# Performance work log

Hardware: AMD Instinct MI355X
Metric: run time of the kernel (lower is better)

Reference implementation:

```python
import jax, jax.numpy as jnp
import numpy as np

N_NODES = 20000
N_EDGES = 200000
D_MODEL = 128
N_HEADS = 8
N_LAYERS = 2  # num_gnn - 1 concat layers


def setup_inputs() -> dict:
    key = jax.random.key(0)
    ks = jax.random.split(key, 12)
    s = 0.05  # keep activations well-scaled across residual layers
    hd = D_MODEL // N_HEADS  # 16
    return {
        "x": jax.random.normal(ks[0], (N_NODES, D_MODEL), jnp.float32),
        "src": jax.random.randint(ks[1], (N_EDGES,), 0, N_NODES),
        "dst": jax.random.randint(ks[2], (N_EDGES,), 0, N_NODES),
        "Ws": jax.random.normal(ks[3], (N_LAYERS, D_MODEL, D_MODEL), jnp.float32) * s,
        "als": jax.random.normal(ks[4], (N_LAYERS, N_HEADS, hd), jnp.float32) * s,
        "ars": jax.random.normal(ks[5], (N_LAYERS, N_HEADS, hd), jnp.float32) * s,
        "bs": jax.random.normal(ks[6], (N_LAYERS, D_MODEL), jnp.float32) * s,
        "W_last": jax.random.normal(ks[7], (D_MODEL, N_HEADS * D_MODEL), jnp.float32) * s,
        "al_last": jax.random.normal(ks[8], (N_HEADS, D_MODEL), jnp.float32) * s,
        "ar_last": jax.random.normal(ks[9], (N_HEADS, D_MODEL), jnp.float32) * s,
        "b_last": jax.random.normal(ks[10], (N_HEADS * D_MODEL,), jnp.float32) * s,
    }


def gat_conv(h, src, dst, W, al, ar, b, num_nodes):
    """DGL GATConv (eval mode, dropout off): returns (N, H, D) head outputs."""
    H, D = al.shape
    feat = (h @ W).reshape(num_nodes, H, D)          # (N,H,D)
    el = jnp.sum(feat * al[None], axis=-1)           # (N,H) attn on src side
    er = jnp.sum(feat * ar[None], axis=-1)           # (N,H) attn on dst side
    e = jax.nn.leaky_relu(el[src] + er[dst], 0.2)    # (E,H)
    # edge softmax over incoming edges of each dst node, per head
    m = jax.ops.segment_max(e, dst, num_segments=num_nodes)  # (N,H)
    p = jnp.exp(e - m[dst])                          # (E,H)
    z = jax.ops.segment_sum(p, dst, num_segments=num_nodes)  # (N,H)
    a = p / z[dst]                                   # (E,H)
    msg = feat[src] * a[..., None]                   # (E,H,D) weighted messages
    rst = jax.ops.segment_sum(msg, dst, num_segments=num_nodes)  # (N,H,D)
    return rst + b.reshape(1, H, D)


def reference(x, src, dst, Ws, als, ars, bs, W_last, al_last, ar_last, b_last):
    N = x.shape[0]
    h = x
    for i in range(N_LAYERS):
        temp = gat_conv(h, src, dst, Ws[i], als[i], ars[i], bs[i], N)  # (N,H,hd)
        h = h + jax.nn.elu(temp.reshape(N, -1))       # concat heads, ELU, residual
    temp = gat_conv(h, src, dst, W_last, al_last, ar_last, b_last, N)  # (N,H,D)
    h = h + jnp.mean(temp, axis=1)                    # mean over heads, residual
    return h
```

## Files before the change

kernel.cpp:

```cpp
#include <hip/hip_runtime.h>
#include <math.h>

#define N_NODES 20000
#define N_EDGES 200000
#define DM 128
#define NH 8

typedef __attribute__((ext_vector_type(8))) short bf16x8;
typedef __attribute__((ext_vector_type(4))) float f32x4;

__device__ __forceinline__ unsigned short f2b(float f) {
  unsigned int u = __float_as_uint(f);
  unsigned int r = (u + 0x7FFFu + ((u >> 16) & 1u)) >> 16;
  return (unsigned short)r;
}
__device__ __forceinline__ float b2f(unsigned short s) {
  return __uint_as_float(((unsigned int)s) << 16);
}

__global__ void scan_deg(const int* __restrict__ deg, int* __restrict__ off,
                         int* __restrict__ cursor) {
  __shared__ int part[1024];
  const int tid = threadIdx.x;
  const int CHUNK = (N_NODES + 1023) / 1024;
  int base = tid * CHUNK;
  int s = 0;
  for (int i = 0; i < CHUNK; ++i) {
    int idx = base + i;
    if (idx < N_NODES) s += deg[idx];
  }
  part[tid] = s;
  __syncthreads();
  for (int ofs = 1; ofs < 1024; ofs <<= 1) {
    int v = (tid >= ofs) ? part[tid - ofs] : 0;
    __syncthreads();
    part[tid] += v;
    __syncthreads();
  }
  int run = (tid > 0) ? part[tid - 1] : 0;
  for (int i = 0; i < CHUNK; ++i) {
    int idx = base + i;
    if (idx < N_NODES) {
      off[idx] = run;
      cursor[idx] = run;
      run += deg[idx];
    }
  }
  if (tid == 0) off[N_NODES] = part[1023];
}

__global__ void scatter_e(const int* __restrict__ src, const int* __restrict__ dst,
                          int* __restrict__ cursor, int* __restrict__ csr_src) {
  int e = blockIdx.x * blockDim.x + threadIdx.x;
  if (e < N_EDGES) {
    int p = atomicAdd(&cursor[dst[e]], 1);
    csr_src[p] = src[e];
  }
}

__global__ void prep_all(const float* __restrict__ x, float* __restrict__ h,
                         unsigned short* __restrict__ hb, const int* __restrict__ dst,
                         int* __restrict__ deg, const float* __restrict__ Ws,
                         unsigned short* __restrict__ wsz, const float* __restrict__ W_last,
                         unsigned short* __restrict__ wpsz, const float* __restrict__ al_last,
                         const float* __restrict__ ar_last, const float* __restrict__ b_last,
                         unsigned short* __restrict__ wlrsz, float* __restrict__ mb) {
  int i = blockIdx.x * blockDim.x + threadIdx.x;
  if (i < N_NODES * DM) {
    float v = x[i];
    h[i] = v;
    hb[i] = f2b(v);
  }
  if (i < N_EDGES) atomicAdd(&deg[dst[i]], 1);
  if (i < 2 * 16384) {
    int layer = i >> 14;
    int r = i & 16383;
    int j = r & 7, l = (r >> 3) & 63, f = (r >> 9) & 7, ks = r >> 12;
    int k = ks * 32 + ((l >> 4) << 3) + j;
    int n = f * 16 + (l & 15);
    wsz[i] = f2b(Ws[(size_t)layer * 16384 + k * 128 + n]);
  }
  if (i < 131072) {
    int j = i & 7, l = (i >> 3) & 63, f = (i >> 9) & 7, ks = i >> 12;
    int k = ks * 32 + ((l >> 4) << 3) + j;
    int n = f * 16 + (l & 15);
    int h_ = k >> 7, ko = k & 127;
    wpsz[i] = f2b(W_last[(size_t)ko * 1024 + h_ * 128 + n] * 0.125f);
  }
  if (i < 2048) {
    int j = i & 7, l = (i >> 3) & 63, ks = i >> 9;
    int k = ks * 32 + ((l >> 4) << 3) + j;
    int n = l & 15;
    int hh = n & 7;
    const float* av = (n < 8) ? (al_last + hh * 128) : (ar_last + hh * 128);
    float s = 0.f;
    for (int d = 0; d < 128; ++d) s += W_last[(size_t)k * 1024 + hh * 128 + d] * av[d];
    wlrsz[i] = f2b(s);
  }
  if (i < 128) {
    float s = 0.f;
#pragma unroll
    for (int hh = 0; hh < 8; ++hh) s += b_last[hh * 128 + i];
    mb[i] = s * 0.125f;
  }
}

template <int K, bool LAST>
__global__ __launch_bounds__(256) void gemm_mfma(
    const unsigned short* __restrict__ A, const unsigned short* __restrict__ Bsz,
    const float* __restrict__ hres, const float* __restrict__ mb,
    unsigned short* __restrict__ Cb, float* __restrict__ Cf,
    const float* __restrict__ al, const float* __restrict__ ar,
    float* __restrict__ elr) {
  const int tid = threadIdx.x;
  const int lane = tid & 63;
  const int wid = tid >> 6;
  const int wrow = wid & 1, wc = wid >> 1;
  const int r0 = blockIdx.x * 32;
  const int arow = r0 + wrow * 16 + (lane & 15);
  const int kg = lane >> 4;

  f32x4 acc[4];
#pragma unroll
  for (int fi = 0; fi < 4; ++fi) acc[fi] = {0.f, 0.f, 0.f, 0.f};

  const bf16x8* Ap = (const bf16x8*)(A + (size_t)arow * K + kg * 8);
  for (int ks = 0; ks < K / 32; ++ks) {
    bf16x8 a = Ap[ks * 4];
#pragma unroll
    for (int fi = 0; fi < 4; ++fi) {
      int f = wc * 4 + fi;
      bf16x8 b = *(const bf16x8*)(Bsz + (((size_t)(ks * 8 + f) * 64 + lane) << 3));
      acc[fi] = __builtin_amdgcn_mfma_f32_16x16x32_bf16(a, b, acc[fi], 0, 0, 0);
    }
  }

  const int rbase = r0 + wrow * 16 + (lane >> 4) * 4;
#pragma unroll
  for (int fi = 0; fi < 4; ++fi) {
    int col = wc * 64 + fi * 16 + (lane & 15);
#pragma unroll
    for (int r = 0; r < 4; ++r) {
      int row = rbase + r;
      float v = acc[fi][r];
      if (LAST)
        Cf[(size_t)row * DM + col] = v + hres[(size_t)row * DM + col] + mb[col];
      else
        Cb[(size_t)row * DM + col] = f2b(v);
    }
  }

  if (!LAST) {
#pragma unroll
    for (int fi = 0; fi < 4; ++fi) {
      int hh = wc * 4 + fi;
      float alv = al[hh * 16 + (lane & 15)];
      float arv = ar[hh * 16 + (lane & 15)];
#pragma unroll
      for (int r = 0; r < 4; ++r) {
        float pl = acc[fi][r] * alv;
        float pr = acc[fi][r] * arv;
#pragma unroll
        for (int msk = 1; msk < 16; msk <<= 1) {
          pl += __shfl_xor(pl, msk, 64);
          pr += __shfl_xor(pr, msk, 64);
        }
        if ((lane & 15) == 0) {
          int row = rbase + r;
          elr[row * 16 + hh] = pl;
          elr[row * 16 + 8 + hh] = pr;
        }
      }
    }
  }
}

__global__ __launch_bounds__(256) void elr_last(const unsigned short* __restrict__ hb,
                                                const unsigned short* __restrict__ wlrsz,
                                                float* __restrict__ elr) {
  const int lane = threadIdx.x & 63;
  const int wid = threadIdx.x >> 6;
  const int r0 = blockIdx.x * 64 + wid * 16;
  const int arow = r0 + (lane & 15);
  const int kg = lane >> 4;
  f32x4 acc = {0.f, 0.f, 0.f, 0.f};
  int arowc = arow < N_NODES ? arow : N_NODES - 1;
  const bf16x8* Ap = (const bf16x8*)(hb + (size_t)arowc * 128 + kg * 8);
#pragma unroll
  for (int ks = 0; ks < 4; ++ks) {
    bf16x8 a = Ap[ks * 4];
    bf16x8 b = *(const bf16x8*)(wlrsz + (((size_t)ks * 64 + lane) << 3));
    acc = __builtin_amdgcn_mfma_f32_16x16x32_bf16(a, b, acc, 0, 0, 0);
  }
  const int col = lane & 15;
  const int rbase = r0 + (lane >> 4) * 4;
#pragma unroll
  for (int r = 0; r < 4; ++r) {
    int row = rbase + r;
    if (row < N_NODES) elr[row * 16 + col] = acc[r];
  }
}

__global__ __launch_bounds__(256) void fused_small(
    const int* __restrict__ off, const int* __restrict__ csr_src,
    const unsigned short* __restrict__ feat, const float* __restrict__ elr,
    const float* __restrict__ bias, float* __restrict__ h, unsigned short* __restrict__ hb) {
  __shared__ float a_lds[4][64];
  __shared__ int s_lds[4][8];
  __shared__ float zi_lds[4][8];
  const int wid = threadIdx.x >> 6;
  const int t = blockIdx.x * 4 + wid;
  const int lane = threadIdx.x & 63;
  const int e_loc = lane >> 3, hh = lane & 7;
  const int h0 = lane >> 4;
  const int beg = off[t], end = off[t + 1];
  const float ert = elr[t * 16 + 8 + hh];

  float z = 0.f, acc0 = 0.f, acc1 = 0.f;
  for (int base = beg; base < end; base += 8) {
    int e = base + e_loc;
    int s = 0;
    float ex = 0.f;
    if (e < end) {
      s = csr_src[e];
      float xv = elr[s * 16 + hh] + ert;
      xv = xv > 0.f ? xv : 0.2f * xv;
      ex = __expf(xv);
    }
    a_lds[wid][lane] = ex;
    if (hh == 0) s_lds[wid][e_loc] = s;
    __builtin_amdgcn_wave_barrier();
    asm volatile("s_waitcnt lgkmcnt(0)" ::: "memory");
    z += ex;
    int n = min(8, end - base);
    for (int e2 = 0; e2 < n; ++e2) {
      int s2 = s_lds[wid][e2];
      float a0 = a_lds[wid][e2 * 8 + h0];
      float a1 = a_lds[wid][e2 * 8 + 4 + h0];
      acc0 += a0 * b2f(feat[(size_t)s2 * 128 + lane]);
      acc1 += a1 * b2f(feat[(size_t)s2 * 128 + 64 + lane]);
    }
    __builtin_amdgcn_wave_barrier();
  }
  z += __shfl_xor(z, 8, 64);
  z += __shfl_xor(z, 16, 64);
  z += __shfl_xor(z, 32, 64);
  if (e_loc == 0) zi_lds[wid][hh] = (z > 0.f) ? 1.f / z : 0.f;
  __builtin_amdgcn_wave_barrier();
  asm volatile("s_waitcnt lgkmcnt(0)" ::: "memory");
  acc0 *= zi_lds[wid][h0];
  acc1 *= zi_lds[wid][h0 + 4];

  float v0 = acc0 + bias[lane];
  float v1 = acc1 + bias[lane + 64];
  v0 = v0 > 0.f ? v0 : expm1f(v0);
  v1 = v1 > 0.f ? v1 : expm1f(v1);
  size_t idx = (size_t)t * 128;
  float nh0 = h[idx + lane] + v0;
  float nh1 = h[idx + lane + 64] + v1;
  h[idx + lane] = nh0;
  h[idx + lane + 64] = nh1;
  hb[idx + lane] = f2b(nh0);
  hb[idx + lane + 64] = f2b(nh1);
}

__global__ __launch_bounds__(256) void fused_last(
    const int* __restrict__ off, const int* __restrict__ csr_src,
    const unsigned short* __restrict__ hb, const float* __restrict__ elr,
    unsigned short* __restrict__ g) {
  __shared__ float a_lds[4][64];
  __shared__ int s_lds[4][8];
  __shared__ float zi_lds[4][8];
  const int wid = threadIdx.x >> 6;
  const int t = blockIdx.x * 4 + wid;
  const int lane = threadIdx.x & 63;
  const int e_loc = lane >> 3, hh = lane & 7;
  const int beg = off[t], end = off[t + 1];
  const float ert = elr[t * 16 + 8 + hh];

  float z = 0.f;
  float accA[8], accB[8];
#pragma unroll
  for (int k = 0; k < 8; ++k) accA[k] = accB[k] = 0.f;

  for (int base = beg; base < end; base += 8) {
    int e = base + e_loc;
    int s = 0;
    float ex = 0.f;
    if (e < end) {
      s = csr_src[e];
      float xv = elr[s * 16 + hh] + ert;
      xv = xv > 0.f ? xv : 0.2f * xv;
      ex = __expf(xv);
    }
    a_lds[wid][lane] = ex;
    if (hh == 0) s_lds[wid][e_loc] = s;
    __builtin_amdgcn_wave_barrier();
    asm volatile("s_waitcnt lgkmcnt(0)" ::: "memory");
    z += ex;
    int n = min(8, end - base);
    for (int e2 = 0; e2 < n; ++e2) {
      int s2 = s_lds[wid][e2];
      float4 pa = *(const float4*)&a_lds[wid][e2 * 8];
      float4 pb = *(const float4*)&a_lds[wid][e2 * 8 + 4];
      float hv0 = b2f(hb[(size_t)s2 * 128 + lane]);
      float hv1 = b2f(hb[(size_t)s2 * 128 + 64 + lane]);
      accA[0] += pa.x * hv0; accB[0] += pa.x * hv1;
      accA[1] += pa.y * hv0; accB[1] += pa.y * hv1;
      accA[2] += pa.z * hv0; accB[2] += pa.z * hv1;
      accA[3] += pa.w * hv0; accB[3] += pa.w * hv1;
      accA[4] += pb.x * hv0; accB[4] += pb.x * hv1;
      accA[5] += pb.y * hv0; accB[5] += pb.y * hv1;
      accA[6] += pb.z * hv0; accB[6] += pb.z * hv1;
      accA[7] += pb.w * hv0; accB[7] += pb.w * hv1;
    }
    __builtin_amdgcn_wave_barrier();
  }
  z += __shfl_xor(z, 8, 64);
  z += __shfl_xor(z, 16, 64);
  z += __shfl_xor(z, 32, 64);
  if (e_loc == 0) zi_lds[wid][hh] = (z > 0.f) ? 1.f / z : 0.f;
  __builtin_amdgcn_wave_barrier();
  asm volatile("s_waitcnt lgkmcnt(0)" ::: "memory");
  float4 zia = *(const float4*)&zi_lds[wid][0];
  float4 zib = *(const float4*)&zi_lds[wid][4];
  float ziv[8] = {zia.x, zia.y, zia.z, zia.w, zib.x, zib.y, zib.z, zib.w};
#pragma unroll
  for (int h2 = 0; h2 < 8; ++h2) {
    g[(size_t)t * 1024 + h2 * 128 + lane] = f2b(accA[h2] * ziv[h2]);
    g[(size_t)t * 1024 + h2 * 128 + 64 + lane] = f2b(accB[h2] * ziv[h2]);
  }
}

extern "C" void kernel_launch(void* const* d_in, const int* in_sizes, int n_in,
                              void* d_out, int out_size, void* d_ws, size_t ws_size,
                              hipStream_t stream) {
  const float* x = (const float*)d_in[0];
  const int* src = (const int*)d_in[1];
  const int* dst = (const int*)d_in[2];
  const float* Ws = (const float*)d_in[3];
  const float* als = (const float*)d_in[4];
  const float* ars = (const float*)d_in[5];
  const float* bs = (const float*)d_in[6];
  const float* W_last = (const float*)d_in[7];
  const float* al_last = (const float*)d_in[8];
  const float* ar_last = (const float*)d_in[9];
  const float* b_last = (const float*)d_in[10];
  float* out = (float*)d_out;

  float* h = (float*)d_ws;
  float* elr = h + 2560000;
  float* mb = elr + 320000;
  unsigned short* hb = (unsigned short*)(mb + 128);
  unsigned short* feat = hb + 2560000;
  unsigned short* g = feat + 2560000;
  unsigned short* wsz = g + 20480000;
  unsigned short* wpsz = wsz + 32768;
  unsigned short* wlrsz = wpsz + 131072;
  int* deg = (int*)(wlrsz + 2048);
  int* off = deg + N_NODES;
  int* cursor = off + N_NODES + 1;
  int* csr_src = cursor + N_NODES;

  const int ND = N_NODES * DM;

  hipMemsetAsync(deg, 0, sizeof(int) * N_NODES, stream);
  prep_all<<<(ND + 255) / 256, 256, 0, stream>>>(x, h, hb, dst, deg, Ws, wsz, W_last, wpsz,
                                                 al_last, ar_last, b_last, wlrsz, mb);
  scan_deg<<<1, 1024, 0, stream>>>(deg, off, cursor);
  scatter_e<<<(N_EDGES + 255) / 256, 256, 0, stream>>>(src, dst, cursor, csr_src);

  const int GB = N_NODES / 32;
  const int FB = N_NODES / 4;
  for (int layer = 0; layer < 2; ++layer) {
    gemm_mfma<DM, false><<<GB, 256, 0, stream>>>(hb, wsz + layer * 16384, nullptr, nullptr,
                                                 feat, nullptr, als + layer * NH * 16,
                                                 ars + layer * NH * 16, elr);
    fused_small<<<FB, 256, 0, stream>>>(off, csr_src, feat, elr, bs + layer * DM, h, hb);
  }

  elr_last<<<(N_NODES + 63) / 64, 256, 0, stream>>>(hb, wlrsz, elr);
  fused_last<<<FB, 256, 0, stream>>>(off, csr_src, hb, elr, g);
  gemm_mfma<NH * DM, true><<<GB, 256, 0, stream>>>(g, wpsz, h, mb, nullptr, out, nullptr,
                                                   nullptr, nullptr);
}
```

Baseline: 201.8 us.

## Fuse last-layer aggregation with output GEMM via LDS tile, drop global g buffer

The last GAT layer's per-node 1024-wide aggregated messages are now staged in an LDS tile of 16 rows per block and multiplied by the projection weights with MFMA in the same kernel. This removes the write and re-read of the roughly 40 MB bf16 intermediate g and one kernel launch, at the cost of fewer blocks and serialized per-wave aggregation of 4 nodes each. The weight preparation is also split from the x conversion, replacing the memset with in-kernel zeroing of deg. The layer aggregation kernels now read two adjacent bf16 features per lane as one 32-bit load, using paired float2 and ushort2 stores.

```diff
diff --git a/kernel.cpp b/kernel.cpp
--- a/kernel.cpp
+++ b/kernel.cpp
@@ -58,20 +58,13 @@
   }
 }
 
-__global__ void prep_all(const float* __restrict__ x, float* __restrict__ h,
-                         unsigned short* __restrict__ hb, const int* __restrict__ dst,
-                         int* __restrict__ deg, const float* __restrict__ Ws,
-                         unsigned short* __restrict__ wsz, const float* __restrict__ W_last,
-                         unsigned short* __restrict__ wpsz, const float* __restrict__ al_last,
-                         const float* __restrict__ ar_last, const float* __restrict__ b_last,
-                         unsigned short* __restrict__ wlrsz, float* __restrict__ mb) {
+__global__ void prep_w(const float* __restrict__ Ws, unsigned short* __restrict__ wsz,
+                       const float* __restrict__ W_last, unsigned short* __restrict__ wpsz,
+                       const float* __restrict__ al_last, const float* __restrict__ ar_last,
+                       const float* __restrict__ b_last, unsigned short* __restrict__ wlrsz,
+                       float* __restrict__ mb, int* __restrict__ deg) {
   int i = blockIdx.x * blockDim.x + threadIdx.x;
-  if (i < N_NODES * DM) {
-    float v = x[i];
-    h[i] = v;
-    hb[i] = f2b(v);
-  }
-  if (i < N_EDGES) atomicAdd(&deg[dst[i]], 1);
+  if (i < N_NODES) deg[i] = 0;
   if (i < 2 * 16384) {
     int layer = i >> 14;
     int r = i & 16383;
@@ -105,13 +98,23 @@
   }
 }
 
-template <int K, bool LAST>
+__global__ void prep_x(const float* __restrict__ x, float* __restrict__ h,
+                       unsigned short* __restrict__ hb, const int* __restrict__ dst,
+                       int* __restrict__ deg) {
+  int i = blockIdx.x * blockDim.x + threadIdx.x;
+  if (i < N_NODES * DM) {
+    float v = x[i];
+    h[i] = v;
+    hb[i] = f2b(v);
+  }
+  if (i < N_EDGES) atomicAdd(&deg[dst[i]], 1);
+}
+
+template <int K>
 __global__ __launch_bounds__(256) void gemm_mfma(
     const unsigned short* __restrict__ A, const unsigned short* __restrict__ Bsz,
-    const float* __restrict__ hres, const float* __restrict__ mb,
-    unsigned short* __restrict__ Cb, float* __restrict__ Cf,
-    const float* __restrict__ al, const float* __restrict__ ar,
-    float* __restrict__ elr) {
+    unsigned short* __restrict__ Cb, const float* __restrict__ al,
+    const float* __restrict__ ar, float* __restrict__ elr) {
   const int tid = threadIdx.x;
   const int lane = tid & 63;
   const int wid = tid >> 6;
@@ -141,35 +144,28 @@
     int col = wc * 64 + fi * 16 + (lane & 15);
 #pragma unroll
     for (int r = 0; r < 4; ++r) {
-      int row = rbase + r;
-      float v = acc[fi][r];
-      if (LAST)
-        Cf[(size_t)row * DM + col] = v + hres[(size_t)row * DM + col] + mb[col];
-      else
-        Cb[(size_t)row * DM + col] = f2b(v);
-    }
-  }
-
-  if (!LAST) {
-#pragma unroll
-    for (int fi = 0; fi < 4; ++fi) {
-      int hh = wc * 4 + fi;
-      float alv = al[hh * 16 + (lane & 15)];
-      float arv = ar[hh * 16 + (lane & 15)];
-#pragma unroll
-      for (int r = 0; r < 4; ++r) {
-        float pl = acc[fi][r] * alv;
-        float pr = acc[fi][r] * arv;
-#pragma unroll
-        for (int msk = 1; msk < 16; msk <<= 1) {
-          pl += __shfl_xor(pl, msk, 64);
-          pr += __shfl_xor(pr, msk, 64);
-        }
-        if ((lane & 15) == 0) {
-          int row = rbase + r;
-          elr[row * 16 + hh] = pl;
-          elr[row * 16 + 8 + hh] = pr;
-        }
+      Cb[(size_t)(rbase + r) * DM + col] = f2b(acc[fi][r]);
+    }
+  }
+
+#pragma unroll
+  for (int fi = 0; fi < 4; ++fi) {
+    int hh = wc * 4 + fi;
+    float alv = al[hh * 16 + (lane & 15)];
+    float arv = ar[hh * 16 + (lane & 15)];
+#pragma unroll
+    for (int r = 0; r < 4; ++r) {
+      float pl = acc[fi][r] * alv;
+      float pr = acc[fi][r] * arv;
+#pragma unroll
+      for (int msk = 1; msk < 16; msk <<= 1) {
+        pl += __shfl_xor(pl, msk, 64);
+        pr += __shfl_xor(pr, msk, 64);
+      }
+      if ((lane & 15) == 0) {
+        int row = rbase + r;
+        elr[row * 16 + hh] = pl;
+        elr[row * 16 + 8 + hh] = pr;
       }
     }
   }
@@ -212,7 +208,7 @@
   const int t = blockIdx.x * 4 + wid;
   const int lane = threadIdx.x & 63;
   const int e_loc = lane >> 3, hh = lane & 7;
-  const int h0 = lane >> 4;
+  const int hg = lane >> 3;
   const int beg = off[t], end = off[t + 1];
   const float ert = elr[t * 16 + 8 + hh];
 
@@ -235,10 +231,10 @@
     int n = min(8, end - base);
     for (int e2 = 0; e2 < n; ++e2) {
       int s2 = s_lds[wid][e2];
-      float a0 = a_lds[wid][e2 * 8 + h0];
-      float a1 = a_lds[wid][e2 * 8 + 4 + h0];
-      acc0 += a0 * b2f(feat[(size_t)s2 * 128 + lane]);
-      acc1 += a1 * b2f(feat[(size_t)s2 * 128 + 64 + lane]);
+      float a = a_lds[wid][e2 * 8 + hg];
+      unsigned int hv = *(const unsigned int*)&feat[(size_t)s2 * 128 + 2 * lane];
+      acc0 += a * b2f((unsigned short)(hv & 0xffffu));
+      acc1 += a * b2f((unsigned short)(hv >> 16));
     }
     __builtin_amdgcn_wave_barrier();
   }
@@ -248,87 +244,120 @@
   if (e_loc == 0) zi_lds[wid][hh] = (z > 0.f) ? 1.f / z : 0.f;
   __builtin_amdgcn_wave_barrier();
   asm volatile("s_waitcnt lgkmcnt(0)" ::: "memory");
-  acc0 *= zi_lds[wid][h0];
-  acc1 *= zi_lds[wid][h0 + 4];
-
-  float v0 = acc0 + bias[lane];
-  float v1 = acc1 + bias[lane + 64];
+  float zi = zi_lds[wid][hg];
+
+  float2 bv = *(const float2*)&bias[2 * lane];
+  float v0 = acc0 * zi + bv.x;
+  float v1 = acc1 * zi + bv.y;
   v0 = v0 > 0.f ? v0 : expm1f(v0);
   v1 = v1 > 0.f ? v1 : expm1f(v1);
-  size_t idx = (size_t)t * 128;
-  float nh0 = h[idx + lane] + v0;
-  float nh1 = h[idx + lane + 64] + v1;
-  h[idx + lane] = nh0;
-  h[idx + lane + 64] = nh1;
-  hb[idx + lane] = f2b(nh0);
-  hb[idx + lane + 64] = f2b(nh1);
-}
-
-__global__ __launch_bounds__(256) void fused_last(
+  size_t idx = (size_t)t * 128 + 2 * lane;
+  float2 hv = *(const float2*)&h[idx];
+  float nh0 = hv.x + v0;
+  float nh1 = hv.y + v1;
+  *(float2*)&h[idx] = make_float2(nh0, nh1);
+  *(ushort2*)&hb[idx] = make_ushort2(f2b(nh0), f2b(nh1));
+}
+
+__global__ __launch_bounds__(256) void agg_gemm_last(
     const int* __restrict__ off, const int* __restrict__ csr_src,
     const unsigned short* __restrict__ hb, const float* __restrict__ elr,
-    unsigned short* __restrict__ g) {
+    const unsigned short* __restrict__ wpsz, const float* __restrict__ hres,
+    const float* __restrict__ mb, float* __restrict__ out) {
+  __shared__ unsigned short gt[16][1032];
   __shared__ float a_lds[4][64];
   __shared__ int s_lds[4][8];
   __shared__ float zi_lds[4][8];
   const int wid = threadIdx.x >> 6;
-  const int t = blockIdx.x * 4 + wid;
   const int lane = threadIdx.x & 63;
+  const int t0 = blockIdx.x * 16;
   const int e_loc = lane >> 3, hh = lane & 7;
-  const int beg = off[t], end = off[t + 1];
-  const float ert = elr[t * 16 + 8 + hh];
-
-  float z = 0.f;
-  float accA[8], accB[8];
-#pragma unroll
-  for (int k = 0; k < 8; ++k) accA[k] = accB[k] = 0.f;
-
-  for (int base = beg; base < end; base += 8) {
-    int e = base + e_loc;
-    int s = 0;
-    float ex = 0.f;
-    if (e < end) {
-      s = csr_src[e];
-      float xv = elr[s * 16 + hh] + ert;
-      xv = xv > 0.f ? xv : 0.2f * xv;
-      ex = __expf(xv);
-    }
-    a_lds[wid][lane] = ex;
-    if (hh == 0) s_lds[wid][e_loc] = s;
+
+  for (int ni = 0; ni < 4; ++ni) {
+    const int r = wid * 4 + ni;
+    const int t = t0 + r;
+    const int beg = off[t], end = off[t + 1];
+    const float ert = elr[t * 16 + 8 + hh];
+    float z = 0.f;
+    float accA[8], accB[8];
+#pragma unroll
+    for (int k = 0; k < 8; ++k) accA[k] = accB[k] = 0.f;
+
+    for (int base = beg; base < end; base += 8) {
+      int e = base + e_loc;
+      int s = 0;
+      float ex = 0.f;
+      if (e < end) {
+        s = csr_src[e];
+        float xv = elr[s * 16 + hh] + ert;
+        xv = xv > 0.f ? xv : 0.2f * xv;
+        ex = __expf(xv);
+      }
+      a_lds[wid][lane] = ex;
+      if (hh == 0) s_lds[wid][e_loc] = s;
+      __builtin_amdgcn_wave_barrier();
+      asm volatile("s_waitcnt lgkmcnt(0)" ::: "memory");
+      z += ex;
+      int n = min(8, end - base);
+      for (int e2 = 0; e2 < n; ++e2) {
+        int s2 = s_lds[wid][e2];
+        float4 pa = *(const float4*)&a_lds[wid][e2 * 8];
+        float4 pb = *(const float4*)&a_lds[wid][e2 * 8 + 4];
+        unsigned int hv = *(const unsigned int*)&hb[(size_t)s2 * 128 + 2 * lane];
+        float h0 = b2f((unsigned short)(hv & 0xffffu));
+        float h1 = b2f((unsigned short)(hv >> 16));
+        accA[0] += pa.x * h0; accB[0] += pa.x * h1;
+        accA[1] += pa.y * h0; accB[1] += pa.y * h1;
+        accA[2] += pa.z * h0; accB[2] += pa.z * h1;
+        accA[3] += pa.w * h0; accB[3] += pa.w * h1;
+        accA[4] += pb.x * h0; accB[4] += pb.x * h1;
+        accA[5] += pb.y * h0; accB[5] += pb.y * h1;
+        accA[6] += pb.z * h0; accB[6] += pb.z * h1;
+        accA[7] += pb.w * h0; accB[7] += pb.w * h1;
+      }
+      __builtin_amdgcn_wave_barrier();
+    }
+    z += __shfl_xor(z, 8, 64);
+    z += __shfl_xor(z, 16, 64);
+    z += __shfl_xor(z, 32, 64);
+    if (e_loc == 0) zi_lds[wid][hh] = (z > 0.f) ? 1.f / z : 0.f;
     __builtin_amdgcn_wave_barrier();
     asm volatile("s_waitcnt lgkmcnt(0)" ::: "memory");
-    z += ex;
-    int n = min(8, end - base);
-    for (int e2 = 0; e2 < n; ++e2) {
-      int s2 = s_lds[wid][e2];
-      float4 pa = *(const float4*)&a_lds[wid][e2 * 8];
-      float4 pb = *(const float4*)&a_lds[wid][e2 * 8 + 4];
-      float hv0 = b2f(hb[(size_t)s2 * 128 + lane]);
-      float hv1 = b2f(hb[(size_t)s2 * 128 + 64 + lane]);
-      accA[0] += pa.x * hv0; accB[0] += pa.x * hv1;
-      accA[1] += pa.y * hv0; accB[1] += pa.y * hv1;
-      accA[2] += pa.z * hv0; accB[2] += pa.z * hv1;
-      accA[3] += pa.w * hv0; accB[3] += pa.w * hv1;
-      accA[4] += pb.x * hv0; accB[4] += pb.x * hv1;
-      accA[5] += pb.y * hv0; accB[5] += pb.y * hv1;
-      accA[6] += pb.z * hv0; accB[6] += pb.z * hv1;
-      accA[7] += pb.w * hv0; accB[7] += pb.w * hv1;
+#pragma unroll
+    for (int h2 = 0; h2 < 8; ++h2) {
+      float zi = zi_lds[wid][h2];
+      *(ushort2*)&gt[r][h2 * 128 + 2 * lane] =
+          make_ushort2(f2b(accA[h2] * zi), f2b(accB[h2] * zi));
     }
     __builtin_amdgcn_wave_barrier();
   }
-  z += __shfl_xor(z, 8, 64);
-  z += __shfl_xor(z, 16, 64);
-  z += __shfl_xor(z, 32, 64);
-  if (e_loc == 0) zi_lds[wid][hh] = (z > 0.f) ? 1.f / z : 0.f;
-  __builtin_amdgcn_wave_barrier();
-  asm volatile("s_waitcnt lgkmcnt(0)" ::: "memory");
-  float4 zia = *(const float4*)&zi_lds[wid][0];
-  float4 zib = *(const float4*)&zi_lds[wid][4];
-  float ziv[8] = {zia.x, zia.y, zia.z, zia.w, zib.x, zib.y, zib.z, zib.w};
-#pragma unroll
-  for (int h2 = 0; h2 < 8; ++h2) {
-    g[(size_t)t * 1024 + h2 * 128 + lane] = f2b(accA[h2] * ziv[h2]);
-    g[(size_t)t * 1024 + h2 * 128 + 64 + lane] = f2b(accB[h2] * ziv[h2]);
+  __syncthreads();
+
+  f32x4 acc2[2];
+  acc2[0] = {0.f, 0.f, 0.f, 0.f};
+  acc2[1] = {0.f, 0.f, 0.f, 0.f};
+  const int ar16 = lane & 15;
+  const int kg = lane >> 4;
+#pragma unroll 4
+  for (int ks = 0; ks < 32; ++ks) {
+    bf16x8 a = *(const bf16x8*)&gt[ar16][ks * 32 + kg * 8];
+#pragma unroll
+    for (int fi = 0; fi < 2; ++fi) {
+      int f = wid * 2 + fi;
+      bf16x8 b = *(const bf16x8*)(wpsz + (((size_t)(ks * 8 + f) * 64 + lane) << 3));
+      acc2[fi] = __builtin_amdgcn_mfma_f32_16x16x32_bf16(a, b, acc2[fi], 0, 0, 0);
+    }
+  }
+  const int rb = (lane >> 4) * 4;
+#pragma unroll
+  for (int fi = 0; fi < 2; ++fi) {
+    int col = wid * 32 + fi * 16 + (lane & 15);
+#pragma unroll
+    for (int r = 0; r < 4; ++r) {
+      int row = t0 + rb + r;
+      out[(size_t)row * 128 + col] =
+          acc2[fi][r] + hres[(size_t)row * 128 + col] + mb[col];
+    }
   }
 }
 
@@ -353,8 +382,7 @@
   float* mb = elr + 320000;
   unsigned short* hb = (unsigned short*)(mb + 128);
   unsigned short* feat = hb + 2560000;
-  unsigned short* g = feat + 2560000;
-  unsigned short* wsz = g + 20480000;
+  unsigned short* wsz = feat + 2560000;
   unsigned short* wpsz = wsz + 32768;
   unsigned short* wlrsz = wpsz + 131072;
   int* deg = (int*)(wlrsz + 2048);
@@ -364,23 +392,20 @@
 
   const int ND = N_NODES * DM;
 
-  hipMemsetAsync(deg, 0, sizeof(int) * N_NODES, stream);
-  prep_all<<<(ND + 255) / 256, 256, 0, stream>>>(x, h, hb, dst, deg, Ws, wsz, W_last, wpsz,
-                                                 al_last, ar_last, b_last, wlrsz, mb);
+  prep_w<<<512, 256, 0, stream>>>(Ws, wsz, W_last, wpsz, al_last, ar_last, b_last, wlrsz,
+                                  mb, deg);
+  prep_x<<<(ND + 255) / 256, 256, 0, stream>>>(x, h, hb, dst, deg);
   scan_deg<<<1, 1024, 0, stream>>>(deg, off, cursor);
   scatter_e<<<(N_EDGES + 255) / 256, 256, 0, stream>>>(src, dst, cursor, csr_src);
 
   const int GB = N_NODES / 32;
   const int FB = N_NODES / 4;
   for (int layer = 0; layer < 2; ++layer) {
-    gemm_mfma<DM, false><<<GB, 256, 0, stream>>>(hb, wsz + layer * 16384, nullptr, nullptr,
-                                                 feat, nullptr, als + layer * NH * 16,
-                                                 ars + layer * NH * 16, elr);
+    gemm_mfma<DM><<<GB, 256, 0, stream>>>(hb, wsz + layer * 16384, feat,
+                                          als + layer * NH * 16, ars + layer * NH * 16, elr);
     fused_small<<<FB, 256, 0, stream>>>(off, csr_src, feat, elr, bs + layer * DM, h, hb);
   }
 
   elr_last<<<(N_NODES + 63) / 64, 256, 0, stream>>>(hb, wlrsz, elr);
-  fused_last<<<FB, 256, 0, stream>>>(off, csr_src, hb, elr, g);
-  gemm_mfma<NH * DM, true><<<GB, 256, 0, stream>>>(g, wpsz, h, mb, nullptr, out, nullptr,
-                                                   nullptr, nullptr);
-}
+  agg_gemm_last<<<N_NODES / 16, 256, 0, stream>>>(off, csr_src, hb, elr, wpsz, h, mb, out);
+}
```

Measured after the change: 215.1 us. 6.6% more time.
